# Performance work log

Hardware: AMD Instinct MI355X
Metric: run time of the kernel (lower is better)

## Reference

```python
import jax, jax.numpy as jnp
import numpy as np

B, S, H = 32, 4096, 16
QC, LORA, ROPE, NOPE, VH, DM = 1536, 512, 64, 128, 128, 2048
SCALE = 1.0 / np.sqrt(NOPE + ROPE)


def _rope(x, pos):
    # GPT-NeoX style rotary, dim=ROPE, base=10000. x: [B,H,ROPE] or [B,ROPE]
    half = ROPE // 2
    inv = 1.0 / (10000.0 ** (jnp.arange(half, dtype=jnp.float32) / half))
    f = pos.astype(jnp.float32)[:, None] * inv  # [B, half]
    cos, sin = jnp.cos(f), jnp.sin(f)
    if x.ndim == 3:
        cos, sin = cos[:, None, :], sin[:, None, :]
    x1, x2 = x[..., :half], x[..., half:]
    return jnp.concatenate([x1 * cos - x2 * sin, x2 * cos + x1 * sin], axis=-1)


def setup_inputs() -> dict:
    key = jax.random.key(0)
    ks = jax.random.split(key, 11)
    w = 0.02  # small init so logits are well-scaled
    return {
        "q_c": jax.random.normal(ks[0], (B, QC), jnp.float32),
        "k_c_normed": jax.random.normal(ks[1], (B, LORA), jnp.float32),
        "k_pe": jax.random.normal(ks[2], (B, ROPE), jnp.float32),
        "kv_c_cache": jax.random.normal(ks[3], (B, S, LORA), jnp.float32),
        "k_pe_cache": jax.random.normal(ks[4], (B, S, ROPE), jnp.float32),
        "W_UQ": jax.random.normal(ks[5], (QC, H, NOPE), jnp.float32) * w,
        "W_UK": jax.random.normal(ks[6], (LORA, H, NOPE), jnp.float32) * w,
        "W_QR": jax.random.normal(ks[7], (QC, H * ROPE), jnp.float32) * w,
        "W_UV": jax.random.normal(ks[8], (LORA, H, VH), jnp.float32) * w,
        "W_O": jax.random.normal(ks[9], (H * VH, DM), jnp.float32) * w,
        "input_positions": jnp.full((B,), S - 1, dtype=jnp.int32),
    }


def reference(q_c, k_c_normed, k_pe, kv_c_cache, k_pe_cache,
              W_UQ, W_UK, W_QR, W_UV, W_O, input_positions):
    pos = input_positions
    # matrix-absorbed q_nope: (q_c @ W_UQ) absorbed through W_UK -> latent space
    q_t = jnp.einsum('bd,dhn->bhn', q_c, W_UQ)            # [B,H,NOPE]
    q_nope = jnp.einsum('bhn,lhn->bhl', q_t, W_UK)        # [B,H,LORA]
    q_pe = _rope((q_c @ W_QR).reshape(B, H, ROPE), pos)   # [B,H,ROPE]
    k_pe_rot = _rope(k_pe, pos)                            # [B,ROPE]
    # write current latent token into cache (paged write flattened)
    b_idx = jnp.arange(B)
    kv_c = kv_c_cache.at[b_idx, pos].set(k_c_normed)       # [B,S,LORA]
    kp = k_pe_cache.at[b_idx, pos].set(k_pe_rot)           # [B,S,ROPE]
    # attention in latent space
    scores = (jnp.einsum('bhl,bsl->bhs', q_nope, kv_c)
              + jnp.einsum('bhr,bsr->bhs', q_pe, kp)) * SCALE
    attn = jax.nn.softmax(scores, axis=-1)                 # [B,H,S]
    o = jnp.einsum('bhs,bsl->bhl', attn, kv_c)             # [B,H,LORA]
    v = jnp.einsum('bhl,lhv->bhv', o, W_UV)                # [B,H,VH]
    out = v.reshape(B, H * VH) @ W_O                       # [B,DM]
    return out.reshape(B, 1, DM)
```

## Files before the change

kernel.cpp:

```cpp
#include <hip/hip_runtime.h>
#include <hip/hip_bf16.h>
#include <math.h>

#define B 32
#define S 4096
#define H 16
#define QC 1536
#define LORA 512
#define ROPE 64
#define NOPE 128
#define VH 128
#define DM 2048
#define NC 32
#define CHUNK (S / NC)
#define TR 8
#define NT (CHUNK / TR)
#define NKS 24

__device__ __constant__ float SCALE_C = 0.07216878364870323f;

__global__ __launch_bounds__(256) void k_proj_part(
    const float* __restrict__ q_c, const float* __restrict__ W_UQ,
    const float* __restrict__ W_QR, float* __restrict__ part) {
    const int ks = blockIdx.x, cs = blockIdx.y, t = threadIdx.x;
    const int k0 = ks * 64;
    __shared__ float qs[64][32];
    for (int i = t; i < 64 * 32; i += 256) {
        const int k = i >> 5, b2 = i & 31;
        qs[k][b2] = q_c[(size_t)b2 * QC + k0 + k];
    }
    __syncthreads();
    const int tc = t & 63, tb = t >> 6;
    const int col = cs * 256 + tc * 4;
    const float* W; int N, coll;
    if (cs < 8) { W = W_UQ; N = 2048; coll = col; }
    else        { W = W_QR; N = 1024; coll = col - 2048; }
    float4 acc[8];
#pragma unroll
    for (int i = 0; i < 8; i++) acc[i] = make_float4(0.f, 0.f, 0.f, 0.f);
#pragma unroll 4
    for (int k = 0; k < 64; ++k) {
        const float4 w4 = *(const float4*)(W + (size_t)(k0 + k) * N + coll);
        const float4 a1 = *(const float4*)&qs[k][tb * 8];
        const float4 a2 = *(const float4*)&qs[k][tb * 8 + 4];
        acc[0].x += a1.x * w4.x; acc[0].y += a1.x * w4.y; acc[0].z += a1.x * w4.z; acc[0].w += a1.x * w4.w;
        acc[1].x += a1.y * w4.x; acc[1].y += a1.y * w4.y; acc[1].z += a1.y * w4.z; acc[1].w += a1.y * w4.w;
        acc[2].x += a1.z * w4.x; acc[2].y += a1.z * w4.y; acc[2].z += a1.z * w4.z; acc[2].w += a1.z * w4.w;
        acc[3].x += a1.w * w4.x; acc[3].y += a1.w * w4.y; acc[3].z += a1.w * w4.z; acc[3].w += a1.w * w4.w;
        acc[4].x += a2.x * w4.x; acc[4].y += a2.x * w4.y; acc[4].z += a2.x * w4.z; acc[4].w += a2.x * w4.w;
        acc[5].x += a2.y * w4.x; acc[5].y += a2.y * w4.y; acc[5].z += a2.y * w4.z; acc[5].w += a2.y * w4.w;
        acc[6].x += a2.z * w4.x; acc[6].y += a2.z * w4.y; acc[6].z += a2.z * w4.z; acc[6].w += a2.z * w4.w;
        acc[7].x += a2.w * w4.x; acc[7].y += a2.w * w4.y; acc[7].z += a2.w * w4.z; acc[7].w += a2.w * w4.w;
    }
#pragma unroll
    for (int j = 0; j < 8; j++) {
        const int b2 = tb * 8 + j;
        *(float4*)(part + ((size_t)ks * 32 + b2) * 3072 + col) = acc[j];
    }
}

__global__ void k_proj_reduce(const float* __restrict__ part, float* __restrict__ q_t,
                              float* __restrict__ qr) {
    const int idx = blockIdx.x * 256 + threadIdx.x;
    const int b = idx / 768, c4 = idx % 768;
    const int col = c4 * 4;
    float4 acc = make_float4(0.f, 0.f, 0.f, 0.f);
    for (int ks = 0; ks < NKS; ks++) {
        const float4 p = *(const float4*)(part + ((size_t)ks * 32 + b) * 3072 + col);
        acc.x += p.x; acc.y += p.y; acc.z += p.z; acc.w += p.w;
    }
    if (col < 2048) *(float4*)(q_t + (size_t)b * 2048 + col) = acc;
    else            *(float4*)(qr + (size_t)b * 1024 + col - 2048) = acc;
}

__global__ void k_rope(const float* __restrict__ qr, const float* __restrict__ k_pe,
                       const int* __restrict__ pos_arr, float* __restrict__ q_pe,
                       float* __restrict__ kpe_rot) {
    const int b = blockIdx.x, t = threadIdx.x;
    const int pos = pos_arr[b];
    for (int p = t; p < (H + 1) * 32; p += 256) {
        const int j = p & 31;
        const int grp = p >> 5;
        const double inv = pow(10000.0, -(double)j / 32.0);
        const double f = (double)pos * inv;
        const float c = (float)cos(f), s = (float)sin(f);
        if (grp < H) {
            const float* x = qr + (size_t)b * 1024 + grp * 64;
            float* o = q_pe + (size_t)b * 1024 + grp * 64;
            const float x1 = x[j], x2 = x[j + 32];
            o[j] = x1 * c - x2 * s;
            o[j + 32] = x2 * c + x1 * s;
        } else {
            const float* x = k_pe + (size_t)b * 64;
            float* o = kpe_rot + (size_t)b * 64;
            const float x1 = x[j], x2 = x[j + 32];
            o[j] = x1 * c - x2 * s;
            o[j + 32] = x2 * c + x1 * s;
        }
    }
}

__global__ __launch_bounds__(256) void k_qnope(
    const float* __restrict__ q_t, const float* __restrict__ W_UK,
    float* __restrict__ q_nope) {
    const int l0 = blockIdx.x * 64, b0 = blockIdx.y * 4, h = blockIdx.z;
    const int t = threadIdx.x;
    __shared__ float qs[4][NOPE];
    for (int i = t; i < 4 * NOPE; i += 256) {
        const int b2 = i >> 7, n = i & 127;
        qs[b2][n] = q_t[(size_t)(b0 + b2) * 2048 + h * NOPE + n];
    }
    __syncthreads();
    const int wave = t >> 6, lane = t & 63;
    const int half = lane >> 5, nl = (lane & 31) * 4;
    for (int sw = 0; sw < 8; ++sw) {
        const int l = l0 + sw * 8 + wave * 2 + half;
        const float4 w4 = *(const float4*)(W_UK + ((size_t)l * H + h) * NOPE + nl);
#pragma unroll
        for (int b2 = 0; b2 < 4; ++b2) {
            const float4 a4 = *(const float4*)&qs[b2][nl];
            float d = a4.x * w4.x + a4.y * w4.y + a4.z * w4.z + a4.w * w4.w;
            d += __shfl_xor(d, 16);
            d += __shfl_xor(d, 8);
            d += __shfl_xor(d, 4);
            d += __shfl_xor(d, 2);
            d += __shfl_xor(d, 1);
            if ((lane & 31) == 0)
                q_nope[((size_t)(b0 + b2) * H + h) * LORA + l] = d;
        }
    }
}

__global__ __launch_bounds__(128) void k_flash(
    const float* __restrict__ q_nope, const float* __restrict__ q_pe,
    const float* __restrict__ kv_cache, const float* __restrict__ kpe_cache,
    const float* __restrict__ k_c_normed, const float* __restrict__ kpe_rot,
    const int* __restrict__ pos_arr, float* __restrict__ part_o,
    float* __restrict__ part_ml) {
    __shared__ float lds_kv[2][TR][LORA];
    __shared__ float lds_pe[2][TR][ROPE];
    const int blk = blockIdx.x;
    const int b = blk / NC, c = blk % NC;
    const int t = threadIdx.x;
    const int g = t >> 4, j = t & 15;
    const int wave = t >> 6, lane = t & 63;
    const int pos = pos_arr[b];
    const int s0 = c * CHUNK;
    const int rel = pos - s0;
    const int ptile = (rel >= 0 && rel < CHUNK) ? (rel / TR) : -1;

    const char* kvg = (const char*)kv_cache + (size_t)b * S * LORA * 4;
    const char* peg = (const char*)kpe_cache + (size_t)b * S * ROPE * 4;
    const float* kc_b = k_c_normed + (size_t)b * LORA;
    const float* kr_b = kpe_rot + (size_t)b * ROPE;

    const int wo = wave * 1024 + lane * 16;

    auto stage = [&](int bi, int tile) {
        const char* gk = kvg + (size_t)(s0 + tile * TR) * (LORA * 4);
        char* lk = (char*)&lds_kv[bi][0][0];
#pragma unroll
        for (int i = 0; i < 8; ++i) {
            __builtin_amdgcn_global_load_lds(
                (const __attribute__((address_space(1))) void*)(gk + i * 2048 + wo),
                (__attribute__((address_space(3))) void*)(lk + i * 2048 + wave * 1024),
                16, 0, 0);
        }
        const char* gp = peg + (size_t)(s0 + tile * TR) * (ROPE * 4);
        char* lp = (char*)&lds_pe[bi][0][0];
        __builtin_amdgcn_global_load_lds(
            (const __attribute__((address_space(1))) void*)(gp + wo),
            (__attribute__((address_space(3))) void*)(lp + wave * 1024),
            16, 0, 0);
    };
    auto patch = [&](int bi, int prow) {
        ((float4*)&lds_kv[bi][prow][0])[t] = ((const float4*)kc_b)[t];
        if (t < 16)
            ((float4*)&lds_pe[bi][prow][0])[t] = ((const float4*)kr_b)[t];
    };

    float4 q4[2][9];
#pragma unroll
    for (int h = 0; h < 2; ++h) {
        const float* qn = q_nope + ((size_t)b * H + 2 * g + h) * LORA;
#pragma unroll
        for (int k = 0; k < 8; k++) q4[h][k] = *(const float4*)(qn + 4 * j + 64 * k);
        q4[h][8] = *(const float4*)(q_pe + ((size_t)b * H + 2 * g + h) * 64 + 4 * j);
    }

    float m_run[2] = {-INFINITY, -INFINITY}, l_run[2] = {0.f, 0.f};
    float4 o_acc[2][8];
#pragma unroll
    for (int h = 0; h < 2; ++h)
#pragma unroll
        for (int k = 0; k < 8; k++) o_acc[h][k] = make_float4(0.f, 0.f, 0.f, 0.f);

    stage(0, 0);
    asm volatile("s_waitcnt vmcnt(0)" ::: "memory");
    __syncthreads();
    if (ptile == 0) { patch(0, rel); __syncthreads(); }

    int cur = 0;
    for (int tile = 0; tile < NT; ++tile) {
        if (tile + 1 < NT) stage(cur ^ 1, tile + 1);

        for (int r = 0; r < TR; ++r) {
            const float* kvr = &lds_kv[cur][r][0];
            float4 kv4[8];
#pragma unroll
            for (int k = 0; k < 8; k++) kv4[k] = *(const float4*)(kvr + 4 * j + 64 * k);
            float4 p4 = *(const float4*)(&lds_pe[cur][r][0] + 4 * j);

            float sc[2];
#pragma unroll
            for (int h = 0; h < 2; ++h) {
                float acc = 0.f;
#pragma unroll
                for (int k = 0; k < 8; k++)
                    acc += q4[h][k].x * kv4[k].x + q4[h][k].y * kv4[k].y +
                           q4[h][k].z * kv4[k].z + q4[h][k].w * kv4[k].w;
                acc += q4[h][8].x * p4.x + q4[h][8].y * p4.y +
                       q4[h][8].z * p4.z + q4[h][8].w * p4.w;
                sc[h] = acc;
            }
#pragma unroll
            for (int msk = 8; msk >= 1; msk >>= 1) {
                sc[0] += __shfl_xor(sc[0], msk);
                sc[1] += __shfl_xor(sc[1], msk);
            }
#pragma unroll
            for (int h = 0; h < 2; ++h) {
                const float s = sc[h] * SCALE_C;
                if (s > m_run[h] + 8.0f) {
                    const float alpha = __expf(m_run[h] - s);
                    l_run[h] *= alpha;
#pragma unroll
                    for (int k = 0; k < 8; k++) {
                        o_acc[h][k].x *= alpha; o_acc[h][k].y *= alpha;
                        o_acc[h][k].z *= alpha; o_acc[h][k].w *= alpha;
                    }
                    m_run[h] = s;
                }
                const float p = __expf(s - m_run[h]);
                l_run[h] += p;
#pragma unroll
                for (int k = 0; k < 8; k++) {
                    o_acc[h][k].x += p * kv4[k].x; o_acc[h][k].y += p * kv4[k].y;
                    o_acc[h][k].z += p * kv4[k].z; o_acc[h][k].w += p * kv4[k].w;
                }
            }
        }

        asm volatile("s_waitcnt vmcnt(0)" ::: "memory");
        __syncthreads();
        if (tile + 1 < NT && ptile == tile + 1) {
            patch(cur ^ 1, rel - ptile * TR);
            __syncthreads();
        }
        cur ^= 1;
    }

    float* po = part_o + (((size_t)b * NC + c) * H) * LORA;
#pragma unroll
    for (int h = 0; h < 2; ++h) {
        float* p = po + (size_t)(2 * g + h) * LORA;
#pragma unroll
        for (int k = 0; k < 8; k++) *(float4*)(p + 4 * j + 64 * k) = o_acc[h][k];
    }
    if (j == 0) {
        float* pml = part_ml + (((size_t)b * NC + c) * H + 2 * g) * 2;
        pml[0] = m_run[0]; pml[1] = l_run[0];
        pml[2] = m_run[1]; pml[3] = l_run[1];
    }
}

__global__ __launch_bounds__(256) void k_combine(
    const float* __restrict__ part_o, const float* __restrict__ part_ml,
    const float* __restrict__ W_UV, float* __restrict__ v) {
    const int b0 = blockIdx.x * 4, h = blockIdx.y, t = threadIdx.x;
    __shared__ float ml_s[4][NC][2];
    __shared__ float o_s[4][LORA];
    if (t < 256) {
        const int b2 = t >> 6, c = (t >> 1) & 31, w = t & 1;
        ml_s[b2][c][w] = part_ml[(((size_t)(b0 + b2) * NC + c) * H + h) * 2 + w];
    }
    __syncthreads();
    float m_b[4], inv_l[4];
#pragma unroll
    for (int b2 = 0; b2 < 4; ++b2) {
        float m = -INFINITY;
        for (int c = 0; c < NC; c++) m = fmaxf(m, ml_s[b2][c][0]);
        float l = 0.f;
        for (int c = 0; c < NC; c++) l += ml_s[b2][c][1] * __expf(ml_s[b2][c][0] - m);
        m_b[b2] = m;
        inv_l[b2] = 1.0f / l;
    }
    for (int i = t; i < 4 * LORA; i += 256) {
        const int b2 = i >> 9, li = i & 511;
        float acc = 0.f;
        for (int c = 0; c < NC; c++) {
            acc += part_o[(((size_t)(b0 + b2) * NC + c) * H + h) * LORA + li] *
                   __expf(ml_s[b2][c][0] - m_b[b2]);
        }
        o_s[b2][li] = acc * inv_l[b2];
    }
    __syncthreads();
    const int vi = t & 127, bp = t >> 7;
    float acc0 = 0.f, acc1 = 0.f;
    for (int l = 0; l < LORA; l += 4) {
        const float w0 = W_UV[(size_t)(l + 0) * (H * VH) + h * VH + vi];
        const float w1 = W_UV[(size_t)(l + 1) * (H * VH) + h * VH + vi];
        const float w2 = W_UV[(size_t)(l + 2) * (H * VH) + h * VH + vi];
        const float w3 = W_UV[(size_t)(l + 3) * (H * VH) + h * VH + vi];
        const float4 oa = *(const float4*)&o_s[bp * 2][l];
        const float4 ob = *(const float4*)&o_s[bp * 2 + 1][l];
        acc0 += oa.x * w0 + oa.y * w1 + oa.z * w2 + oa.w * w3;
        acc1 += ob.x * w0 + ob.y * w1 + ob.z * w2 + ob.w * w3;
    }
    v[(size_t)(b0 + bp * 2) * (H * VH) + h * VH + vi] = acc0;
    v[(size_t)(b0 + bp * 2 + 1) * (H * VH) + h * VH + vi] = acc1;
}

__global__ void k_out(const float* __restrict__ v, const float* __restrict__ W_O,
                      float* __restrict__ out_part) {
    const int dsl = blockIdx.x, ksl = blockIdx.y, t = threadIdx.x;
    const int d0 = dsl * 128, k0 = ksl * 128;
    __shared__ float vs[32][128];
    for (int i = t; i < 32 * 128; i += 256) {
        const int bi = i >> 7, kk = i & 127;
        vs[bi][kk] = v[(size_t)bi * DM + k0 + kk];
    }
    __syncthreads();
    const int dl = t & 127, bh = t >> 7;
    float acc[16];
#pragma unroll
    for (int i = 0; i < 16; i++) acc[i] = 0.f;
    for (int kk = 0; kk < 128; kk += 4) {
        const float w0 = W_O[(size_t)(k0 + kk + 0) * DM + d0 + dl];
        const float w1 = W_O[(size_t)(k0 + kk + 1) * DM + d0 + dl];
        const float w2 = W_O[(size_t)(k0 + kk + 2) * DM + d0 + dl];
        const float w3 = W_O[(size_t)(k0 + kk + 3) * DM + d0 + dl];
#pragma unroll
        for (int i = 0; i < 16; i++) {
            const float4 vv = *(const float4*)&vs[bh * 16 + i][kk];
            acc[i] += vv.x * w0 + vv.y * w1 + vv.z * w2 + vv.w * w3;
        }
    }
    float* op = out_part + (size_t)ksl * 32 * DM;
#pragma unroll
    for (int i = 0; i < 16; i++) op[(size_t)(bh * 16 + i) * DM + d0 + dl] = acc[i];
}

__global__ void k_out_reduce(const float* __restrict__ out_part, float* __restrict__ out) {
    const int idx = blockIdx.x * 256 + threadIdx.x;
    float4 acc = make_float4(0.f, 0.f, 0.f, 0.f);
    for (int ks = 0; ks < 16; ks++) {
        float4 p = *(const float4*)(out_part + (size_t)ks * (32 * DM) + (size_t)idx * 4);
        acc.x += p.x; acc.y += p.y; acc.z += p.z; acc.w += p.w;
    }
    *(float4*)(out + (size_t)idx * 4) = acc;
}

extern "C" void kernel_launch(void* const* d_in, const int* in_sizes, int n_in,
                              void* d_out, int out_size, void* d_ws, size_t ws_size,
                              hipStream_t stream) {
    const float* q_c        = (const float*)d_in[0];
    const float* k_c_normed = (const float*)d_in[1];
    const float* k_pe       = (const float*)d_in[2];
    const float* kv_c_cache = (const float*)d_in[3];
    const float* k_pe_cache = (const float*)d_in[4];
    const float* W_UQ       = (const float*)d_in[5];
    const float* W_UK       = (const float*)d_in[6];
    const float* W_QR       = (const float*)d_in[7];
    const float* W_UV       = (const float*)d_in[8];
    const float* W_O        = (const float*)d_in[9];
    const int*   pos        = (const int*)d_in[10];

    float* ws = (float*)d_ws;
    float* q_t      = ws;
    float* qr       = q_t + 65536;
    float* q_pe     = qr + 32768;
    float* kpe_rot  = q_pe + 32768;
    float* q_nope   = kpe_rot + 2048;
    float* part_o   = q_nope + 262144;
    float* part_ml  = part_o + (size_t)B * NC * H * LORA;
    float* v        = part_ml + (size_t)B * NC * H * 2;
    float* out_part = v + 65536;
    float* proj_part = out_part + (size_t)16 * 32 * DM;

    k_proj_part<<<dim3(NKS, 12), 256, 0, stream>>>(q_c, W_UQ, W_QR, proj_part);
    k_proj_reduce<<<96, 256, 0, stream>>>(proj_part, q_t, qr);
    k_rope<<<32, 256, 0, stream>>>(qr, k_pe, pos, q_pe, kpe_rot);
    k_qnope<<<dim3(8, 8, 16), 256, 0, stream>>>(q_t, W_UK, q_nope);
    k_flash<<<B * NC, 128, 0, stream>>>(q_nope, q_pe, kv_c_cache, k_pe_cache,
                                        k_c_normed, kpe_rot, pos, part_o, part_ml);
    k_combine<<<dim3(8, 16), 256, 0, stream>>>(part_o, part_ml, W_UV, v);
    k_out<<<dim3(16, 16), 256, 0, stream>>>(v, W_O, out_part);
    k_out_reduce<<<64, 256, 0, stream>>>(out_part, (float*)d_out);
}
```

Baseline: 214.8 us.

## Fuse proj-reduce with rope, batch qnope over all B, load KV directly to registers

Merges the projection reduce and rope kernels into one finalize kernel, which saves one launch and the qr round trip. The q_nope kernel now handles all 32 batches per block, so each W_UK element is read once instead of eight times. The flash kernel drops the LDS double buffer built on global_load_lds and instead loads each KV row straight into registers with two-row software prefetch, substituting the current token by pointer selection. Each thread now issues uncoalesced 16-byte global loads, and with only two rows prefetched the kernel may not hide memory latency as well as the previous async copies into shared memory.

```diff
diff --git a/kernel.cpp b/kernel.cpp
--- a/kernel.cpp
+++ b/kernel.cpp
@@ -13,8 +13,6 @@
 #define DM 2048
 #define NC 32
 #define CHUNK (S / NC)
-#define TR 8
-#define NT (CHUNK / TR)
 #define NKS 24
 
 __device__ __constant__ float SCALE_C = 0.07216878364870323f;
@@ -59,43 +57,58 @@
     }
 }
 
-__global__ void k_proj_reduce(const float* __restrict__ part, float* __restrict__ q_t,
-                              float* __restrict__ qr) {
-    const int idx = blockIdx.x * 256 + threadIdx.x;
-    const int b = idx / 768, c4 = idx % 768;
-    const int col = c4 * 4;
-    float4 acc = make_float4(0.f, 0.f, 0.f, 0.f);
-    for (int ks = 0; ks < NKS; ks++) {
-        const float4 p = *(const float4*)(part + ((size_t)ks * 32 + b) * 3072 + col);
-        acc.x += p.x; acc.y += p.y; acc.z += p.z; acc.w += p.w;
-    }
-    if (col < 2048) *(float4*)(q_t + (size_t)b * 2048 + col) = acc;
-    else            *(float4*)(qr + (size_t)b * 1024 + col - 2048) = acc;
-}
-
-__global__ void k_rope(const float* __restrict__ qr, const float* __restrict__ k_pe,
-                       const int* __restrict__ pos_arr, float* __restrict__ q_pe,
-                       float* __restrict__ kpe_rot) {
-    const int b = blockIdx.x, t = threadIdx.x;
-    const int pos = pos_arr[b];
-    for (int p = t; p < (H + 1) * 32; p += 256) {
-        const int j = p & 31;
-        const int grp = p >> 5;
-        const double inv = pow(10000.0, -(double)j / 32.0);
-        const double f = (double)pos * inv;
-        const float c = (float)cos(f), s = (float)sin(f);
-        if (grp < H) {
-            const float* x = qr + (size_t)b * 1024 + grp * 64;
-            float* o = q_pe + (size_t)b * 1024 + grp * 64;
-            const float x1 = x[j], x2 = x[j + 32];
-            o[j] = x1 * c - x2 * s;
-            o[j + 32] = x2 * c + x1 * s;
-        } else {
-            const float* x = k_pe + (size_t)b * 64;
-            float* o = kpe_rot + (size_t)b * 64;
-            const float x1 = x[j], x2 = x[j + 32];
-            o[j] = x1 * c - x2 * s;
-            o[j + 32] = x2 * c + x1 * s;
+__global__ __launch_bounds__(256) void k_finalize(
+    const float* __restrict__ part, const float* __restrict__ k_pe,
+    const int* __restrict__ pos_arr, float* __restrict__ q_t,
+    float* __restrict__ q_pe, float* __restrict__ kpe_rot) {
+    const int blk = blockIdx.x, t = threadIdx.x;
+    if (blk < 64) {
+        const int idx = blk * 256 + t;
+        const int b = idx >> 9, c4 = idx & 511;
+        const int col = c4 * 4;
+        float4 acc = make_float4(0.f, 0.f, 0.f, 0.f);
+        for (int ks = 0; ks < NKS; ks++) {
+            const float4 p = *(const float4*)(part + ((size_t)ks * 32 + b) * 3072 + col);
+            acc.x += p.x; acc.y += p.y; acc.z += p.z; acc.w += p.w;
+        }
+        *(float4*)(q_t + (size_t)b * 2048 + col) = acc;
+    } else if (blk < 80) {
+        const int idx = (blk - 64) * 256 + t;
+        const int b = idx >> 7, rest = idx & 127;
+        const int h = rest >> 3, pr = rest & 7;
+        const int col1 = 2048 + h * 64 + pr * 4;
+        float x1[4] = {0.f, 0.f, 0.f, 0.f}, x2[4] = {0.f, 0.f, 0.f, 0.f};
+        for (int ks = 0; ks < NKS; ks++) {
+            const float* p = part + ((size_t)ks * 32 + b) * 3072;
+            const float4 a = *(const float4*)(p + col1);
+            const float4 c = *(const float4*)(p + col1 + 32);
+            x1[0] += a.x; x1[1] += a.y; x1[2] += a.z; x1[3] += a.w;
+            x2[0] += c.x; x2[1] += c.y; x2[2] += c.z; x2[3] += c.w;
+        }
+        const int pos = pos_arr[b];
+        float o1[4], o2[4];
+#pragma unroll
+        for (int e = 0; e < 4; ++e) {
+            const int j = pr * 4 + e;
+            const double inv = pow(10000.0, -(double)j / 32.0);
+            const double f = (double)pos * inv;
+            const float cc = (float)cos(f), ss = (float)sin(f);
+            o1[e] = x1[e] * cc - x2[e] * ss;
+            o2[e] = x2[e] * cc + x1[e] * ss;
+        }
+        float* qp = q_pe + (size_t)b * 1024 + h * 64 + pr * 4;
+        *(float4*)qp = make_float4(o1[0], o1[1], o1[2], o1[3]);
+        *(float4*)(qp + 32) = make_float4(o2[0], o2[1], o2[2], o2[3]);
+    } else {
+        for (int i = t; i < 32 * 32; i += 256) {
+            const int b = i >> 5, j = i & 31;
+            const int pos = pos_arr[b];
+            const double inv = pow(10000.0, -(double)j / 32.0);
+            const double f = (double)pos * inv;
+            const float cc = (float)cos(f), ss = (float)sin(f);
+            const float x1 = k_pe[(size_t)b * 64 + j], x2 = k_pe[(size_t)b * 64 + j + 32];
+            kpe_rot[(size_t)b * 64 + j] = x1 * cc - x2 * ss;
+            kpe_rot[(size_t)b * 64 + j + 32] = x2 * cc + x1 * ss;
         }
     }
 }
@@ -103,12 +116,12 @@
 __global__ __launch_bounds__(256) void k_qnope(
     const float* __restrict__ q_t, const float* __restrict__ W_UK,
     float* __restrict__ q_nope) {
-    const int l0 = blockIdx.x * 64, b0 = blockIdx.y * 4, h = blockIdx.z;
+    const int l0 = blockIdx.x * 64, h = blockIdx.y;
     const int t = threadIdx.x;
-    __shared__ float qs[4][NOPE];
-    for (int i = t; i < 4 * NOPE; i += 256) {
+    __shared__ float qs[32][NOPE];
+    for (int i = t; i < 32 * NOPE; i += 256) {
         const int b2 = i >> 7, n = i & 127;
-        qs[b2][n] = q_t[(size_t)(b0 + b2) * 2048 + h * NOPE + n];
+        qs[b2][n] = q_t[(size_t)b2 * 2048 + h * NOPE + n];
     }
     __syncthreads();
     const int wave = t >> 6, lane = t & 63;
@@ -116,8 +129,7 @@
     for (int sw = 0; sw < 8; ++sw) {
         const int l = l0 + sw * 8 + wave * 2 + half;
         const float4 w4 = *(const float4*)(W_UK + ((size_t)l * H + h) * NOPE + nl);
-#pragma unroll
-        for (int b2 = 0; b2 < 4; ++b2) {
+        for (int b2 = 0; b2 < 32; ++b2) {
             const float4 a4 = *(const float4*)&qs[b2][nl];
             float d = a4.x * w4.x + a4.y * w4.y + a4.z * w4.z + a4.w * w4.w;
             d += __shfl_xor(d, 16);
@@ -126,7 +138,7 @@
             d += __shfl_xor(d, 2);
             d += __shfl_xor(d, 1);
             if ((lane & 31) == 0)
-                q_nope[((size_t)(b0 + b2) * H + h) * LORA + l] = d;
+                q_nope[((size_t)b2 * H + h) * LORA + l] = d;
         }
     }
 }
@@ -137,48 +149,17 @@
     const float* __restrict__ k_c_normed, const float* __restrict__ kpe_rot,
     const int* __restrict__ pos_arr, float* __restrict__ part_o,
     float* __restrict__ part_ml) {
-    __shared__ float lds_kv[2][TR][LORA];
-    __shared__ float lds_pe[2][TR][ROPE];
     const int blk = blockIdx.x;
     const int b = blk / NC, c = blk % NC;
     const int t = threadIdx.x;
     const int g = t >> 4, j = t & 15;
-    const int wave = t >> 6, lane = t & 63;
     const int pos = pos_arr[b];
-    const int s0 = c * CHUNK;
-    const int rel = pos - s0;
-    const int ptile = (rel >= 0 && rel < CHUNK) ? (rel / TR) : -1;
-
-    const char* kvg = (const char*)kv_cache + (size_t)b * S * LORA * 4;
-    const char* peg = (const char*)kpe_cache + (size_t)b * S * ROPE * 4;
+
+    const float* kv_b = kv_cache + (size_t)b * S * LORA;
+    const float* kp_b = kpe_cache + (size_t)b * S * ROPE;
     const float* kc_b = k_c_normed + (size_t)b * LORA;
     const float* kr_b = kpe_rot + (size_t)b * ROPE;
 
-    const int wo = wave * 1024 + lane * 16;
-
-    auto stage = [&](int bi, int tile) {
-        const char* gk = kvg + (size_t)(s0 + tile * TR) * (LORA * 4);
-        char* lk = (char*)&lds_kv[bi][0][0];
-#pragma unroll
-        for (int i = 0; i < 8; ++i) {
-            __builtin_amdgcn_global_load_lds(
-                (const __attribute__((address_space(1))) void*)(gk + i * 2048 + wo),
-                (__attribute__((address_space(3))) void*)(lk + i * 2048 + wave * 1024),
-                16, 0, 0);
-        }
-        const char* gp = peg + (size_t)(s0 + tile * TR) * (ROPE * 4);
-        char* lp = (char*)&lds_pe[bi][0][0];
-        __builtin_amdgcn_global_load_lds(
-            (const __attribute__((address_space(1))) void*)(gp + wo),
-            (__attribute__((address_space(3))) void*)(lp + wave * 1024),
-            16, 0, 0);
-    };
-    auto patch = [&](int bi, int prow) {
-        ((float4*)&lds_kv[bi][prow][0])[t] = ((const float4*)kc_b)[t];
-        if (t < 16)
-            ((float4*)&lds_pe[bi][prow][0])[t] = ((const float4*)kr_b)[t];
-    };
-
     float4 q4[2][9];
 #pragma unroll
     for (int h = 0; h < 2; ++h) {
@@ -195,69 +176,63 @@
 #pragma unroll
         for (int k = 0; k < 8; k++) o_acc[h][k] = make_float4(0.f, 0.f, 0.f, 0.f);
 
-    stage(0, 0);
-    asm volatile("s_waitcnt vmcnt(0)" ::: "memory");
-    __syncthreads();
-    if (ptile == 0) { patch(0, rel); __syncthreads(); }
-
-    int cur = 0;
-    for (int tile = 0; tile < NT; ++tile) {
-        if (tile + 1 < NT) stage(cur ^ 1, tile + 1);
-
-        for (int r = 0; r < TR; ++r) {
-            const float* kvr = &lds_kv[cur][r][0];
-            float4 kv4[8];
-#pragma unroll
-            for (int k = 0; k < 8; k++) kv4[k] = *(const float4*)(kvr + 4 * j + 64 * k);
-            float4 p4 = *(const float4*)(&lds_pe[cur][r][0] + 4 * j);
-
-            float sc[2];
-#pragma unroll
-            for (int h = 0; h < 2; ++h) {
-                float acc = 0.f;
-#pragma unroll
-                for (int k = 0; k < 8; k++)
-                    acc += q4[h][k].x * kv4[k].x + q4[h][k].y * kv4[k].y +
-                           q4[h][k].z * kv4[k].z + q4[h][k].w * kv4[k].w;
-                acc += q4[h][8].x * p4.x + q4[h][8].y * p4.y +
-                       q4[h][8].z * p4.z + q4[h][8].w * p4.w;
-                sc[h] = acc;
+    const int s0 = c * CHUNK;
+
+    auto load_row = [&](int s, float4* kv, float4& pe) {
+        const float* kvr = (s == pos) ? kc_b : (kv_b + (size_t)s * LORA);
+        const float* per = (s == pos) ? kr_b : (kp_b + (size_t)s * ROPE);
+#pragma unroll
+        for (int k = 0; k < 8; k++) kv[k] = *(const float4*)(kvr + 4 * j + 64 * k);
+        pe = *(const float4*)(per + 4 * j);
+    };
+    auto compute_row = [&](const float4* kv, const float4& p4) {
+        float sc[2];
+#pragma unroll
+        for (int h = 0; h < 2; ++h) {
+            float acc = 0.f;
+#pragma unroll
+            for (int k = 0; k < 8; k++)
+                acc += q4[h][k].x * kv[k].x + q4[h][k].y * kv[k].y +
+                       q4[h][k].z * kv[k].z + q4[h][k].w * kv[k].w;
+            acc += q4[h][8].x * p4.x + q4[h][8].y * p4.y +
+                   q4[h][8].z * p4.z + q4[h][8].w * p4.w;
+            sc[h] = acc;
+        }
+#pragma unroll
+        for (int msk = 8; msk >= 1; msk >>= 1) {
+            sc[0] += __shfl_xor(sc[0], msk);
+            sc[1] += __shfl_xor(sc[1], msk);
+        }
+#pragma unroll
+        for (int h = 0; h < 2; ++h) {
+            const float s = sc[h] * SCALE_C;
+            if (s > m_run[h] + 8.0f) {
+                const float alpha = __expf(m_run[h] - s);
+                l_run[h] *= alpha;
+#pragma unroll
+                for (int k = 0; k < 8; k++) {
+                    o_acc[h][k].x *= alpha; o_acc[h][k].y *= alpha;
+                    o_acc[h][k].z *= alpha; o_acc[h][k].w *= alpha;
+                }
+                m_run[h] = s;
             }
-#pragma unroll
-            for (int msk = 8; msk >= 1; msk >>= 1) {
-                sc[0] += __shfl_xor(sc[0], msk);
-                sc[1] += __shfl_xor(sc[1], msk);
+            const float p = __expf(s - m_run[h]);
+            l_run[h] += p;
+#pragma unroll
+            for (int k = 0; k < 8; k++) {
+                o_acc[h][k].x += p * kv[k].x; o_acc[h][k].y += p * kv[k].y;
+                o_acc[h][k].z += p * kv[k].z; o_acc[h][k].w += p * kv[k].w;
             }
-#pragma unroll
-            for (int h = 0; h < 2; ++h) {
-                const float s = sc[h] * SCALE_C;
-                if (s > m_run[h] + 8.0f) {
-                    const float alpha = __expf(m_run[h] - s);
-                    l_run[h] *= alpha;
-#pragma unroll
-                    for (int k = 0; k < 8; k++) {
-                        o_acc[h][k].x *= alpha; o_acc[h][k].y *= alpha;
-                        o_acc[h][k].z *= alpha; o_acc[h][k].w *= alpha;
-                    }
-                    m_run[h] = s;
-                }
-                const float p = __expf(s - m_run[h]);
-                l_run[h] += p;
-#pragma unroll
-                for (int k = 0; k < 8; k++) {
-                    o_acc[h][k].x += p * kv4[k].x; o_acc[h][k].y += p * kv4[k].y;
-                    o_acc[h][k].z += p * kv4[k].z; o_acc[h][k].w += p * kv4[k].w;
-                }
-            }
-        }
-
-        asm volatile("s_waitcnt vmcnt(0)" ::: "memory");
-        __syncthreads();
-        if (tile + 1 < NT && ptile == tile + 1) {
-            patch(cur ^ 1, rel - ptile * TR);
-            __syncthreads();
-        }
-        cur ^= 1;
+        }
+    };
+
+    float4 kvA[8], kvB[8], peA, peB;
+    load_row(s0, kvA, peA);
+    for (int r = 0; r < CHUNK; r += 2) {
+        load_row(s0 + r + 1, kvB, peB);
+        compute_row(kvA, peA);
+        if (r + 2 < CHUNK) load_row(s0 + r + 2, kvA, peA);
+        compute_row(kvB, peB);
     }
 
     float* po = part_o + (((size_t)b * NC + c) * H) * LORA;
@@ -378,8 +353,8 @@
 
     float* ws = (float*)d_ws;
     float* q_t      = ws;
-    float* qr       = q_t + 65536;
-    float* q_pe     = qr + 32768;
+    float* qr_unused= q_t + 65536;
+    float* q_pe     = qr_unused + 32768;
     float* kpe_rot  = q_pe + 32768;
     float* q_nope   = kpe_rot + 2048;
     float* part_o   = q_nope + 262144;
@@ -389,9 +364,8 @@
     float* proj_part = out_part + (size_t)16 * 32 * DM;
 
     k_proj_part<<<dim3(NKS, 12), 256, 0, stream>>>(q_c, W_UQ, W_QR, proj_part);
-    k_proj_reduce<<<96, 256, 0, stream>>>(proj_part, q_t, qr);
-    k_rope<<<32, 256, 0, stream>>>(qr, k_pe, pos, q_pe, kpe_rot);
-    k_qnope<<<dim3(8, 8, 16), 256, 0, stream>>>(q_t, W_UK, q_nope);
+    k_finalize<<<81, 256, 0, stream>>>(proj_part, k_pe, pos, q_t, q_pe, kpe_rot);
+    k_qnope<<<dim3(8, 16), 256, 0, stream>>>(q_t, W_UK, q_nope);
     k_flash<<<B * NC, 128, 0, stream>>>(q_nope, q_pe, kv_c_cache, k_pe_cache,
                                         k_c_normed, kpe_rot, pos, part_o, part_ml);
     k_combine<<<dim3(8, 16), 256, 0, stream>>>(part_o, part_ml, W_UV, v);
```

Measured after the change: 352.5 us. 64.1% more time.
